# Performance work log

Hardware: AMD Instinct MI355X
Metric: run time of the kernel (lower is better)

Reference implementation:

```python
import jax, jax.numpy as jnp
import numpy as np

COMMITMENT_COST = 0.25
NUM_EMBEDDINGS = 4096
EMBEDDING_DIM = 256


def setup_inputs() -> dict:
    key = jax.random.key(0)
    k1, k2 = jax.random.split(key)
    inputs = jax.random.normal(k1, (32, EMBEDDING_DIM, 2048), dtype=jnp.float32)
    # nn.Embedding weight initialized uniform(-1/K, 1/K)
    codebook = jax.random.uniform(
        k2, (NUM_EMBEDDINGS, EMBEDDING_DIM), dtype=jnp.float32,
        minval=-1.0 / NUM_EMBEDDINGS, maxval=1.0 / NUM_EMBEDDINGS)
    return {"inputs": inputs, "codebook": codebook}


def reference(inputs, codebook):
    B, D, S = inputs.shape
    sg = jax.lax.stop_gradient
    # [B, D, S] -> [B*S, D]
    flat = jnp.transpose(inputs, (0, 2, 1)).reshape(-1, D)
    distances = (jnp.sum(flat ** 2, axis=1, keepdims=True)
                 + jnp.sum(codebook ** 2, axis=1)
                 - 2.0 * flat @ codebook.T)
    encoding_indices = jnp.argmin(distances, axis=1)  # [N]
    # direct gather (same math as one-hot @ codebook)
    quantized = codebook[encoding_indices].reshape(B, S, D)
    quantized = jnp.transpose(quantized, (0, 2, 1))  # [B, D, S]
    e_latent_loss = jnp.mean((sg(quantized) - inputs) ** 2)
    q_latent_loss = jnp.mean((quantized - sg(inputs)) ** 2)
    loss = COMMITMENT_COST * e_latent_loss + q_latent_loss
    # straight-through estimator
    quantized_st = inputs + sg(quantized - inputs)
    return quantized_st, loss
```

## Files before the change

### kernel.cpp

```cpp
#include <hip/hip_runtime.h>

#define K_CODES 4096
#define DIM 256
#define SEQ 2048
#define NTOK 65536

typedef __bf16 bf16x8 __attribute__((ext_vector_type(8)));
typedef float floatx4 __attribute__((ext_vector_type(4)));
typedef unsigned short u16x8 __attribute__((ext_vector_type(8)));

__device__ __forceinline__ unsigned short f2bf(float f) {
    union { float f; unsigned int u; } v; v.f = f;
    unsigned int u = v.u;
    unsigned int r = u + 0x7fffu + ((u >> 16) & 1u);
    return (unsigned short)(r >> 16);
}

__device__ __forceinline__ void async_cp16(const void* g, const void* lds_base) {
    typedef __attribute__((address_space(1))) const unsigned int guint;
    typedef __attribute__((address_space(3))) unsigned int luint;
    __builtin_amdgcn_global_load_lds(
        (guint*)(unsigned long long)g,
        (luint*)(unsigned int)(unsigned long long)lds_base,
        16, 0, 0);
}

__global__ __launch_bounds__(256) void k_prep(const float* __restrict__ cb,
        unsigned short* __restrict__ cb_swz, float* __restrict__ norms,
        float* __restrict__ loss_slot) {
    const int c = blockIdx.x;
    const int t = threadIdx.x;
    const int row_loc = t >> 3;
    const int ks = t & 7;
    const int row = c * 32 + row_loc;
    const float* src = cb + (size_t)row * DIM + ks * 32;
    float vals[32];
    float s = 0.0f;
    #pragma unroll
    for (int i = 0; i < 8; ++i) {
        floatx4 v = *(const floatx4*)(src + i * 4);
        #pragma unroll
        for (int j = 0; j < 4; ++j) { vals[i * 4 + j] = v[j]; s += v[j] * v[j]; }
    }
    const int ns = row_loc >> 4, col = row_loc & 15;
    #pragma unroll
    for (int quad = 0; quad < 4; ++quad) {
        u16x8 p;
        #pragma unroll
        for (int j = 0; j < 8; ++j) p[j] = f2bf(vals[quad * 8 + j]);
        *(u16x8*)(cb_swz + ((size_t)((c * 16 + ns * 8 + ks) * 64 + quad * 16 + col)) * 8) = p;
    }
    s += __shfl_xor(s, 1); s += __shfl_xor(s, 2); s += __shfl_xor(s, 4);
    if (ks == 0) norms[row] = s + 0.25f;
    if (c == 0 && t == 0) *loss_slot = 0.0f;
}

__global__ __launch_bounds__(256, 2) void k_argmin(const float* __restrict__ x,
        const unsigned short* __restrict__ cb_swz, const float* __restrict__ norms,
        unsigned int* __restrict__ halfmin, float* __restrict__ loss_slot) {
    __shared__ __align__(16) unsigned short xs[64 * 264];
    __shared__ __align__(16) unsigned short ring[2][8192];
    __shared__ float wpart[4];
    const int t = threadIdx.x;
    const int lane = t & 63, w = t >> 6;
    const int col = lane & 15, quad = lane >> 4;
    const int bx = blockIdx.x;
    const int h = bx & 1;
    const int tb = (bx >> 1) * 256;
    const int b = tb >> 11, s0 = tb & 2047;
    const float* xin = x + (size_t)b * DIM * SEQ;

    {
        const char* src = (const char*)cb_swz + (size_t)h * 64 * 16384;
        #pragma unroll
        for (int i = 0; i < 4; ++i)
            async_cp16(src + i * 4096 + w * 1024 + lane * 16,
                       (char*)ring[0] + i * 4096 + w * 1024);
    }

    bf16x8 af[4][8];
    float a2 = 0.0f;
    const int dg = t >> 4, sq = (t & 15) * 4;
    for (int ph = 0; ph < 4; ++ph) {
        const int sbase = s0 + ph * 64 + sq;
        for (int i = 0; i < 16; ++i) {
            int d = i * 16 + dg;
            floatx4 v = *(const floatx4*)(xin + (size_t)d * SEQ + sbase);
            a2 += v[0]*v[0] + v[1]*v[1] + v[2]*v[2] + v[3]*v[3];
            #pragma unroll
            for (int j = 0; j < 4; ++j) xs[(sq + j) * 264 + d] = f2bf(-2.0f * v[j]);
        }
        __syncthreads();
        if (w == ph) {
            #pragma unroll
            for (int m = 0; m < 4; ++m)
                #pragma unroll
                for (int ks = 0; ks < 8; ++ks)
                    af[m][ks] = *(const bf16x8*)&xs[(m * 16 + col) * 264
                                                    + quad * 8 + ks * 32];
        }
        __syncthreads();
    }
    #pragma unroll
    for (int off = 1; off < 64; off <<= 1) a2 += __shfl_xor(a2, off);
    if (lane == 0) wpart[w] = a2;
    __syncthreads();
    if (t == 0 && h == 0)
        atomicAdd(loss_slot,
                  (wpart[0] + wpart[1] + wpart[2] + wpart[3]) * (1.25f / 16777216.0f));

    unsigned int minkey[4][4];
    #pragma unroll
    for (int m = 0; m < 4; ++m)
        #pragma unroll
        for (int r = 0; r < 4; ++r) minkey[m][r] = 0xFFFFFFFFu;

    #pragma unroll 1
    for (int c = 0; c < 64; ++c) {
        __syncthreads();
        if (c < 63) {
            const char* src = (const char*)cb_swz + (size_t)(h * 64 + c + 1) * 16384;
            char* dst = (char*)ring[(c + 1) & 1];
            #pragma unroll
            for (int i = 0; i < 4; ++i)
                async_cp16(src + i * 4096 + w * 1024 + lane * 16,
                           dst + i * 4096 + w * 1024);
        }
        const unsigned short* buf = ring[c & 1];
        #pragma unroll
        for (int ns = 0; ns < 2; ++ns) {
            const float nv = norms[(h * 64 + c) * 32 + ns * 16 + col];
            bf16x8 bfrag[8];
            #pragma unroll
            for (int ks = 0; ks < 8; ++ks)
                bfrag[ks] = *(const bf16x8*)&buf[((ns * 8 + ks) * 64 + lane) * 8];
            floatx4 acc[4];
            #pragma unroll
            for (int m = 0; m < 4; ++m) acc[m] = (floatx4){nv, nv, nv, nv};
            #pragma unroll
            for (int ks = 0; ks < 8; ++ks)
                #pragma unroll
                for (int m = 0; m < 4; ++m)
                    acc[m] = __builtin_amdgcn_mfma_f32_16x16x32_bf16(
                                 af[m][ks], bfrag[ks], acc[m], 0, 0, 0);
            const unsigned int code = (unsigned int)((h * 64 + c) * 32 + ns * 16 + col);
            #pragma unroll
            for (int m = 0; m < 4; ++m)
                #pragma unroll
                for (int r = 0; r < 4; ++r) {
                    unsigned int key = (__float_as_uint(acc[m][r]) & 0xFFFFF000u) | code;
                    minkey[m][r] = key < minkey[m][r] ? key : minkey[m][r];
                }
        }
    }

    #pragma unroll
    for (int m = 0; m < 4; ++m)
        #pragma unroll
        for (int r = 0; r < 4; ++r) {
            unsigned int k = minkey[m][r];
            #pragma unroll
            for (int off = 8; off >= 1; off >>= 1) {
                unsigned int o = __shfl_xor(k, off);
                k = o < k ? o : k;
            }
            if (col == 0)
                halfmin[h * NTOK + tb + w * 64 + m * 16 + quad * 4 + r] = k;
        }
}

__global__ __launch_bounds__(256) void k_gather(const float* __restrict__ cb,
        const unsigned int* __restrict__ halfmin, float* __restrict__ out,
        float* __restrict__ loss_slot) {
    __shared__ int sidx[64];
    const int t = threadIdx.x;
    const int tb = blockIdx.x * 64;
    const int b = tb >> 11, s0 = tb & 2047;
    if (t < 64) {
        unsigned int k0 = halfmin[tb + t], k1 = halfmin[NTOK + tb + t];
        unsigned int km = k0 < k1 ? k0 : k1;
        sidx[t] = (int)(km & 0xFFFu);
        float dv = __uint_as_float(km & 0xFFFFF000u) - 0.25f;
        #pragma unroll
        for (int off = 32; off; off >>= 1) dv += __shfl_xor(dv, off);
        if (t == 0) atomicAdd(loss_slot, dv * (1.25f / 16777216.0f));
    }
    __syncthreads();
    const int q = t & 15, dg = t >> 4;
    int rows[4];
    #pragma unroll
    for (int k = 0; k < 4; ++k) rows[k] = sidx[q * 4 + k];
    #pragma unroll
    for (int i = 0; i < 16; ++i) {
        const int d = i * 16 + dg;
        floatx4 v;
        #pragma unroll
        for (int k = 0; k < 4; ++k) v[k] = cb[(size_t)rows[k] * DIM + d];
        *(floatx4*)(out + (size_t)b * DIM * SEQ + (size_t)d * SEQ + s0 + q * 4) = v;
    }
}

extern "C" void kernel_launch(void* const* d_in, const int* in_sizes, int n_in,
                              void* d_out, int out_size, void* d_ws, size_t ws_size,
                              hipStream_t stream) {
    const float* inputs   = (const float*)d_in[0];
    const float* codebook = (const float*)d_in[1];
    float* out = (float*)d_out;
    unsigned short* cb_swz = (unsigned short*)d_ws;
    float* norms = (float*)((char*)d_ws + (size_t)K_CODES * DIM * 2);
    unsigned int* halfmin = (unsigned int*)((char*)d_ws + (size_t)K_CODES * DIM * 2
                                            + K_CODES * 4);
    float* loss_slot = out + (out_size - 1);

    hipLaunchKernelGGL(k_prep,   dim3(K_CODES / 32),     dim3(256), 0, stream,
                       codebook, cb_swz, norms, loss_slot);
    hipLaunchKernelGGL(k_argmin, dim3(NTOK / 256 * 2),   dim3(256), 0, stream,
                       inputs, cb_swz, norms, halfmin, loss_slot);
    hipLaunchKernelGGL(k_gather, dim3(NTOK / 64),        dim3(256), 0, stream,
                       codebook, halfmin, out, loss_slot);
}
```

Measured before the change: 259.8 us.

## Triple-buffer codebook ring with split barriers and staged norms in LDS

Replaces the double-buffered codebook ring in the argmin kernel with a three-stage ring that has two chunks in flight. Explicit vmcnt waits and raw s_barrier calls replace the per-iteration __syncthreads, and s_setprio raises priority around the MFMA blocks. Norms are staged once into shared memory, and the -2x staging tile is halved and XOR-swizzled to cut LDS bank conflicts. The goals are better overlap of global-to-LDS loads with MFMA work and less barrier stall, at the cost of more LDS use and fragile hand-written waitcnt logic.

```diff
diff --git a/kernel.cpp b/kernel.cpp
--- a/kernel.cpp
+++ b/kernel.cpp
@@ -58,8 +58,9 @@
 __global__ __launch_bounds__(256, 2) void k_argmin(const float* __restrict__ x,
         const unsigned short* __restrict__ cb_swz, const float* __restrict__ norms,
         unsigned int* __restrict__ halfmin, float* __restrict__ loss_slot) {
-    __shared__ __align__(16) unsigned short xs[64 * 264];
-    __shared__ __align__(16) unsigned short ring[2][8192];
+    __shared__ __align__(16) unsigned short xs[32 * 264];
+    __shared__ __align__(16) unsigned short ring3[3][8192];
+    __shared__ __align__(16) float norms_s[2048];
     __shared__ float wpart[4];
     const int t = threadIdx.x;
     const int lane = t & 63, w = t >> 6;
@@ -73,31 +74,45 @@
     {
         const char* src = (const char*)cb_swz + (size_t)h * 64 * 16384;
         #pragma unroll
-        for (int i = 0; i < 4; ++i)
-            async_cp16(src + i * 4096 + w * 1024 + lane * 16,
-                       (char*)ring[0] + i * 4096 + w * 1024);
+        for (int cc = 0; cc < 2; ++cc)
+            #pragma unroll
+            for (int i = 0; i < 4; ++i)
+                async_cp16(src + cc * 16384 + i * 4096 + w * 1024 + lane * 16,
+                           (char*)ring3[cc] + i * 4096 + w * 1024);
+    }
+    {
+        const float* ng = norms + h * 2048;
+        *(floatx4*)&norms_s[t * 8]     = *(const floatx4*)(ng + t * 8);
+        *(floatx4*)&norms_s[t * 8 + 4] = *(const floatx4*)(ng + t * 8 + 4);
     }
 
     bf16x8 af[4][8];
     float a2 = 0.0f;
-    const int dg = t >> 4, sq = (t & 15) * 4;
-    for (int ph = 0; ph < 4; ++ph) {
-        const int sbase = s0 + ph * 64 + sq;
-        for (int i = 0; i < 16; ++i) {
-            int d = i * 16 + dg;
+    const int q = t & 7, dgp = t >> 3, sq = q * 4;
+    for (int p = 0; p < 8; ++p) {
+        const int sbase = s0 + p * 32 + sq;
+        #pragma unroll
+        for (int i = 0; i < 8; ++i) {
+            const int d = i * 32 + dgp;
             floatx4 v = *(const floatx4*)(xin + (size_t)d * SEQ + sbase);
             a2 += v[0]*v[0] + v[1]*v[1] + v[2]*v[2] + v[3]*v[3];
-            #pragma unroll
-            for (int j = 0; j < 4; ++j) xs[(sq + j) * 264 + d] = f2bf(-2.0f * v[j]);
+            const int chs = (d >> 3) ^ q;
+            #pragma unroll
+            for (int j = 0; j < 4; ++j)
+                xs[(sq + j) * 264 + chs * 8 + (d & 7)] = f2bf(-2.0f * v[j]);
         }
         __syncthreads();
-        if (w == ph) {
-            #pragma unroll
-            for (int m = 0; m < 4; ++m)
+        if ((p >> 1) == w) {
+            const int mm = (p & 1) * 2;
+            #pragma unroll
+            for (int m2 = 0; m2 < 2; ++m2) {
+                const int row = m2 * 16 + col;
+                const int swz = (row >> 2) & 7;
                 #pragma unroll
                 for (int ks = 0; ks < 8; ++ks)
-                    af[m][ks] = *(const bf16x8*)&xs[(m * 16 + col) * 264
-                                                    + quad * 8 + ks * 32];
+                    af[mm + m2][ks] = *(const bf16x8*)
+                        &xs[row * 264 + ((quad + ks * 4) ^ swz) * 8];
+            }
         }
         __syncthreads();
     }
@@ -115,43 +130,77 @@
         #pragma unroll
         for (int r = 0; r < 4; ++r) minkey[m][r] = 0xFFFFFFFFu;
 
+    const unsigned short* rcur = ring3[0];
+    const unsigned short* rnxt = ring3[1];
+    const unsigned short* rstg = ring3[2];
+    const char* srcp = (const char*)cb_swz + ((size_t)h * 64 + 2) * 16384;
+    const float* np = norms_s + col;
+    unsigned int codev = (unsigned int)(h * 64 * 32 + col);
+
     #pragma unroll 1
     for (int c = 0; c < 64; ++c) {
-        __syncthreads();
-        if (c < 63) {
-            const char* src = (const char*)cb_swz + (size_t)(h * 64 + c + 1) * 16384;
-            char* dst = (char*)ring[(c + 1) & 1];
+        float nv0 = np[0];
+        bf16x8 bf0[8];
+        #pragma unroll
+        for (int ks = 0; ks < 8; ++ks)
+            bf0[ks] = *(const bf16x8*)&rcur[(ks * 64 + lane) * 8];
+        if (c < 62) {
             #pragma unroll
             for (int i = 0; i < 4; ++i)
-                async_cp16(src + i * 4096 + w * 1024 + lane * 16,
-                           dst + i * 4096 + w * 1024);
-        }
-        const unsigned short* buf = ring[c & 1];
-        #pragma unroll
-        for (int ns = 0; ns < 2; ++ns) {
-            const float nv = norms[(h * 64 + c) * 32 + ns * 16 + col];
-            bf16x8 bfrag[8];
-            #pragma unroll
-            for (int ks = 0; ks < 8; ++ks)
-                bfrag[ks] = *(const bf16x8*)&buf[((ns * 8 + ks) * 64 + lane) * 8];
-            floatx4 acc[4];
-            #pragma unroll
-            for (int m = 0; m < 4; ++m) acc[m] = (floatx4){nv, nv, nv, nv};
-            #pragma unroll
-            for (int ks = 0; ks < 8; ++ks)
-                #pragma unroll
-                for (int m = 0; m < 4; ++m)
-                    acc[m] = __builtin_amdgcn_mfma_f32_16x16x32_bf16(
-                                 af[m][ks], bfrag[ks], acc[m], 0, 0, 0);
-            const unsigned int code = (unsigned int)((h * 64 + c) * 32 + ns * 16 + col);
+                async_cp16(srcp + i * 4096 + w * 1024 + lane * 16,
+                           (const char*)rstg + i * 4096 + w * 1024);
+        }
+        __builtin_amdgcn_s_barrier();
+        asm volatile("s_waitcnt lgkmcnt(0)" ::: "memory");
+        __builtin_amdgcn_s_setprio(1);
+        floatx4 acc0[4];
+        #pragma unroll
+        for (int m = 0; m < 4; ++m) acc0[m] = (floatx4){nv0, nv0, nv0, nv0};
+        #pragma unroll
+        for (int ks = 0; ks < 8; ++ks)
             #pragma unroll
             for (int m = 0; m < 4; ++m)
-                #pragma unroll
-                for (int r = 0; r < 4; ++r) {
-                    unsigned int key = (__float_as_uint(acc[m][r]) & 0xFFFFF000u) | code;
-                    minkey[m][r] = key < minkey[m][r] ? key : minkey[m][r];
-                }
-        }
+                acc0[m] = __builtin_amdgcn_mfma_f32_16x16x32_bf16(
+                              af[m][ks], bf0[ks], acc0[m], 0, 0, 0);
+        __builtin_amdgcn_s_setprio(0);
+        float nv1 = np[16];
+        bf16x8 bf1[8];
+        #pragma unroll
+        for (int ks = 0; ks < 8; ++ks)
+            bf1[ks] = *(const bf16x8*)&rcur[((8 + ks) * 64 + lane) * 8];
+        #pragma unroll
+        for (int m = 0; m < 4; ++m)
+            #pragma unroll
+            for (int r = 0; r < 4; ++r) {
+                unsigned int key = (__float_as_uint(acc0[m][r]) & 0xFFFFF000u) | codev;
+                minkey[m][r] = key < minkey[m][r] ? key : minkey[m][r];
+            }
+        __builtin_amdgcn_s_barrier();
+        asm volatile("s_waitcnt lgkmcnt(0)" ::: "memory");
+        __builtin_amdgcn_s_setprio(1);
+        floatx4 acc1[4];
+        #pragma unroll
+        for (int m = 0; m < 4; ++m) acc1[m] = (floatx4){nv1, nv1, nv1, nv1};
+        #pragma unroll
+        for (int ks = 0; ks < 8; ++ks)
+            #pragma unroll
+            for (int m = 0; m < 4; ++m)
+                acc1[m] = __builtin_amdgcn_mfma_f32_16x16x32_bf16(
+                              af[m][ks], bf1[ks], acc1[m], 0, 0, 0);
+        __builtin_amdgcn_s_setprio(0);
+        #pragma unroll
+        for (int m = 0; m < 4; ++m)
+            #pragma unroll
+            for (int r = 0; r < 4; ++r) {
+                unsigned int key = (__float_as_uint(acc1[m][r]) & 0xFFFFF000u)
+                                   | (codev + 16);
+                minkey[m][r] = key < minkey[m][r] ? key : minkey[m][r];
+            }
+        if (c < 62) asm volatile("s_waitcnt vmcnt(4)" ::: "memory");
+        else        asm volatile("s_waitcnt vmcnt(0)" ::: "memory");
+        __builtin_amdgcn_s_barrier();
+        const unsigned short* tmp = rcur; rcur = rnxt; rnxt = rstg; rstg = tmp;
+        srcp += 16384; np += 32; codev += 32;
     }
 
     #pragma unroll
```

Result: slower. 282.3 us (+8.6%).

## Switch argmin to 32x32x16 MFMA with swizzled LDS, norms in LDS, staged gather

Applied to the files above, without the earlier changes.

The distance kernel moves from 16x16x32 to 32x32x16 bf16 MFMA tiles. The codebook swizzle and the per-wave A fragments (two 32-token tiles) are rebuilt to match, and the x staging buffer in LDS gets XOR swizzling to avoid bank conflicts. Codebook norms are preloaded into LDS, the block index is remapped so the two codebook halves are scheduled apart, and MFMA sections are raised with s_setprio. The gather kernel now stages whole codebook rows in LDS for coalesced reads before the transposed write. The larger tiles cut LDS B-fragment traffic per FLOP, at the cost of more registers per wave and more complex index mapping.

```diff
diff --git a/kernel.cpp b/kernel.cpp
--- a/kernel.cpp
+++ b/kernel.cpp
@@ -7,6 +7,8 @@
 
 typedef __bf16 bf16x8 __attribute__((ext_vector_type(8)));
 typedef float floatx4 __attribute__((ext_vector_type(4)));
+typedef float floatx2 __attribute__((ext_vector_type(2)));
+typedef float floatx16 __attribute__((ext_vector_type(16)));
 typedef unsigned short u16x8 __attribute__((ext_vector_type(8)));
 
 __device__ __forceinline__ unsigned short f2bf(float f) {
@@ -28,12 +30,12 @@
 __global__ __launch_bounds__(256) void k_prep(const float* __restrict__ cb,
         unsigned short* __restrict__ cb_swz, float* __restrict__ norms,
         float* __restrict__ loss_slot) {
-    const int c = blockIdx.x;
+    const int gc = blockIdx.x;
     const int t = threadIdx.x;
-    const int row_loc = t >> 3;
-    const int ks = t & 7;
-    const int row = c * 32 + row_loc;
-    const float* src = cb + (size_t)row * DIM + ks * 32;
+    const int colc = t >> 3;
+    const int o = t & 7;
+    const int row = gc * 32 + colc;
+    const float* src = cb + (size_t)row * DIM + o * 32;
     float vals[32];
     float s = 0.0f;
     #pragma unroll
@@ -42,31 +44,34 @@
         #pragma unroll
         for (int j = 0; j < 4; ++j) { vals[i * 4 + j] = v[j]; s += v[j] * v[j]; }
     }
-    const int ns = row_loc >> 4, col = row_loc & 15;
-    #pragma unroll
-    for (int quad = 0; quad < 4; ++quad) {
+    #pragma unroll
+    for (int q4 = 0; q4 < 4; ++q4) {
+        const int g8 = o * 4 + q4;
+        const int ks = g8 >> 1, kh = g8 & 1;
         u16x8 p;
         #pragma unroll
-        for (int j = 0; j < 8; ++j) p[j] = f2bf(vals[quad * 8 + j]);
-        *(u16x8*)(cb_swz + ((size_t)((c * 16 + ns * 8 + ks) * 64 + quad * 16 + col)) * 8) = p;
+        for (int j = 0; j < 8; ++j) p[j] = f2bf(vals[q4 * 8 + j]);
+        *(u16x8*)(cb_swz + ((size_t)(gc * 16 + ks) * 64 + kh * 32 + colc) * 8) = p;
     }
     s += __shfl_xor(s, 1); s += __shfl_xor(s, 2); s += __shfl_xor(s, 4);
-    if (ks == 0) norms[row] = s + 0.25f;
-    if (c == 0 && t == 0) *loss_slot = 0.0f;
+    if (o == 0) norms[row] = s + 0.25f;
+    if (gc == 0 && t == 0) *loss_slot = 0.0f;
 }
 
 __global__ __launch_bounds__(256, 2) void k_argmin(const float* __restrict__ x,
         const unsigned short* __restrict__ cb_swz, const float* __restrict__ norms,
         unsigned int* __restrict__ halfmin, float* __restrict__ loss_slot) {
-    __shared__ __align__(16) unsigned short xs[64 * 264];
+    __shared__ __align__(16) unsigned short xs[32 * 264];
     __shared__ __align__(16) unsigned short ring[2][8192];
+    __shared__ __align__(16) float norms_s[2048];
     __shared__ float wpart[4];
     const int t = threadIdx.x;
     const int lane = t & 63, w = t >> 6;
-    const int col = lane & 15, quad = lane >> 4;
-    const int bx = blockIdx.x;
-    const int h = bx & 1;
-    const int tb = (bx >> 1) * 256;
+    const int col32 = lane & 31, kh = lane >> 5;
+    const int bid = blockIdx.x;
+    const int tbid = (bid & 7) * 32 + (bid >> 4);
+    const int h = (bid >> 3) & 1;
+    const int tb = tbid * 256;
     const int b = tb >> 11, s0 = tb & 2047;
     const float* xin = x + (size_t)b * DIM * SEQ;
 
@@ -77,27 +82,43 @@
             async_cp16(src + i * 4096 + w * 1024 + lane * 16,
                        (char*)ring[0] + i * 4096 + w * 1024);
     }
-
-    bf16x8 af[4][8];
+    {
+        const float* ng = norms + h * 2048;
+        *(floatx4*)&norms_s[t * 8]     = *(const floatx4*)(ng + t * 8);
+        *(floatx4*)&norms_s[t * 8 + 4] = *(const floatx4*)(ng + t * 8 + 4);
+    }
+
+    bf16x8 af0[16], af1[16];
     float a2 = 0.0f;
-    const int dg = t >> 4, sq = (t & 15) * 4;
-    for (int ph = 0; ph < 4; ++ph) {
-        const int sbase = s0 + ph * 64 + sq;
-        for (int i = 0; i < 16; ++i) {
-            int d = i * 16 + dg;
+    const int q = t & 7, dgp = t >> 3, sq = q * 4;
+    #pragma unroll
+    for (int p = 0; p < 8; ++p) {
+        const int sbase = s0 + p * 32 + sq;
+        #pragma unroll
+        for (int i = 0; i < 8; ++i) {
+            const int d = i * 32 + dgp;
             floatx4 v = *(const floatx4*)(xin + (size_t)d * SEQ + sbase);
             a2 += v[0]*v[0] + v[1]*v[1] + v[2]*v[2] + v[3]*v[3];
-            #pragma unroll
-            for (int j = 0; j < 4; ++j) xs[(sq + j) * 264 + d] = f2bf(-2.0f * v[j]);
-        }
-        __syncthreads();
-        if (w == ph) {
-            #pragma unroll
-            for (int m = 0; m < 4; ++m)
+            const int chs = (d >> 3) ^ q;
+            #pragma unroll
+            for (int j = 0; j < 4; ++j)
+                xs[(sq + j) * 264 + chs * 8 + (d & 7)] = f2bf(-2.0f * v[j]);
+        }
+        __syncthreads();
+        if ((p >> 1) == w) {
+            const int tok = col32;
+            const int swz = tok >> 2;
+            if ((p & 1) == 0) {
                 #pragma unroll
-                for (int ks = 0; ks < 8; ++ks)
-                    af[m][ks] = *(const bf16x8*)&xs[(m * 16 + col) * 264
-                                                    + quad * 8 + ks * 32];
+                for (int ks = 0; ks < 16; ++ks)
+                    af0[ks] = *(const bf16x8*)
+                        &xs[tok * 264 + ((ks * 2 + kh) ^ swz) * 8];
+            } else {
+                #pragma unroll
+                for (int ks = 0; ks < 16; ++ks)
+                    af1[ks] = *(const bf16x8*)
+                        &xs[tok * 264 + ((ks * 2 + kh) ^ swz) * 8];
+            }
         }
         __syncthreads();
     }
@@ -109,69 +130,77 @@
         atomicAdd(loss_slot,
                   (wpart[0] + wpart[1] + wpart[2] + wpart[3]) * (1.25f / 16777216.0f));
 
-    unsigned int minkey[4][4];
-    #pragma unroll
-    for (int m = 0; m < 4; ++m)
-        #pragma unroll
-        for (int r = 0; r < 4; ++r) minkey[m][r] = 0xFFFFFFFFu;
+    unsigned int minkey0[16], minkey1[16];
+    #pragma unroll
+    for (int r = 0; r < 16; ++r) { minkey0[r] = 0xFFFFFFFFu; minkey1[r] = 0xFFFFFFFFu; }
 
     #pragma unroll 1
     for (int c = 0; c < 64; ++c) {
         __syncthreads();
         if (c < 63) {
-            const char* src = (const char*)cb_swz + (size_t)(h * 64 + c + 1) * 16384;
+            const char* srcp = (const char*)cb_swz + ((size_t)(h * 64) + c + 1) * 16384;
             char* dst = (char*)ring[(c + 1) & 1];
             #pragma unroll
             for (int i = 0; i < 4; ++i)
-                async_cp16(src + i * 4096 + w * 1024 + lane * 16,
+                async_cp16(srcp + i * 4096 + w * 1024 + lane * 16,
                            dst + i * 4096 + w * 1024);
         }
         const unsigned short* buf = ring[c & 1];
-        #pragma unroll
-        for (int ns = 0; ns < 2; ++ns) {
-            const float nv = norms[(h * 64 + c) * 32 + ns * 16 + col];
-            bf16x8 bfrag[8];
-            #pragma unroll
-            for (int ks = 0; ks < 8; ++ks)
-                bfrag[ks] = *(const bf16x8*)&buf[((ns * 8 + ks) * 64 + lane) * 8];
-            floatx4 acc[4];
-            #pragma unroll
-            for (int m = 0; m < 4; ++m) acc[m] = (floatx4){nv, nv, nv, nv};
-            #pragma unroll
-            for (int ks = 0; ks < 8; ++ks)
-                #pragma unroll
-                for (int m = 0; m < 4; ++m)
-                    acc[m] = __builtin_amdgcn_mfma_f32_16x16x32_bf16(
-                                 af[m][ks], bfrag[ks], acc[m], 0, 0, 0);
-            const unsigned int code = (unsigned int)((h * 64 + c) * 32 + ns * 16 + col);
-            #pragma unroll
-            for (int m = 0; m < 4; ++m)
-                #pragma unroll
-                for (int r = 0; r < 4; ++r) {
-                    unsigned int key = (__float_as_uint(acc[m][r]) & 0xFFFFF000u) | code;
-                    minkey[m][r] = key < minkey[m][r] ? key : minkey[m][r];
-                }
-        }
-    }
-
-    #pragma unroll
-    for (int m = 0; m < 4; ++m)
-        #pragma unroll
-        for (int r = 0; r < 4; ++r) {
-            unsigned int k = minkey[m][r];
-            #pragma unroll
-            for (int off = 8; off >= 1; off >>= 1) {
-                unsigned int o = __shfl_xor(k, off);
-                k = o < k ? o : k;
+        const float nv = norms_s[c * 32 + col32];
+        floatx16 acc0, acc1;
+        #pragma unroll
+        for (int r = 0; r < 16; ++r) { acc0[r] = nv; acc1[r] = nv; }
+        #pragma unroll
+        for (int hf = 0; hf < 2; ++hf) {
+            bf16x8 bfr[8];
+            #pragma unroll
+            for (int kk = 0; kk < 8; ++kk)
+                bfr[kk] = *(const bf16x8*)&buf[((hf * 8 + kk) * 64 + lane) * 8];
+            __builtin_amdgcn_s_setprio(1);
+            #pragma unroll
+            for (int kk = 0; kk < 8; ++kk) {
+                acc0 = __builtin_amdgcn_mfma_f32_32x32x16_bf16(
+                           af0[hf * 8 + kk], bfr[kk], acc0, 0, 0, 0);
+                acc1 = __builtin_amdgcn_mfma_f32_32x32x16_bf16(
+                           af1[hf * 8 + kk], bfr[kk], acc1, 0, 0, 0);
             }
-            if (col == 0)
-                halfmin[h * NTOK + tb + w * 64 + m * 16 + quad * 4 + r] = k;
-        }
+            __builtin_amdgcn_s_setprio(0);
+        }
+        const unsigned int code = (unsigned int)((h * 64 + c) * 32) | (unsigned int)col32;
+        #pragma unroll
+        for (int r = 0; r < 16; ++r) {
+            unsigned int k0 = (__float_as_uint(acc0[r]) & 0xFFFFF000u) | code;
+            minkey0[r] = k0 < minkey0[r] ? k0 : minkey0[r];
+            unsigned int k1 = (__float_as_uint(acc1[r]) & 0xFFFFF000u) | code;
+            minkey1[r] = k1 < minkey1[r] ? k1 : minkey1[r];
+        }
+    }
+
+    #pragma unroll
+    for (int r = 0; r < 16; ++r) {
+        unsigned int k = minkey0[r];
+        #pragma unroll
+        for (int off = 16; off >= 1; off >>= 1) {
+            unsigned int o = __shfl_xor(k, off);
+            k = o < k ? o : k;
+        }
+        if (col32 == 0)
+            halfmin[h * NTOK + tb + w * 64 + (r & 3) + 8 * (r >> 2) + 4 * kh] = k;
+        unsigned int k2 = minkey1[r];
+        #pragma unroll
+        for (int off = 16; off >= 1; off >>= 1) {
+            unsigned int o = __shfl_xor(k2, off);
+            k2 = o < k2 ? o : k2;
+        }
+        if (col32 == 0)
+            halfmin[h * NTOK + tb + w * 64 + 32 + (r & 3) + 8 * (r >> 2) + 4 * kh] = k2;
+    }
 }
 
 __global__ __launch_bounds__(256) void k_gather(const float* __restrict__ cb,
         const unsigned int* __restrict__ halfmin, float* __restrict__ out,
         float* __restrict__ loss_slot) {
+    __shared__ float rows_s[32 * 258];
     __shared__ int sidx[64];
     const int t = threadIdx.x;
     const int tb = blockIdx.x * 64;
@@ -186,17 +215,26 @@
         if (t == 0) atomicAdd(loss_slot, dv * (1.25f / 16777216.0f));
     }
     __syncthreads();
-    const int q = t & 15, dg = t >> 4;
-    int rows[4];
-    #pragma unroll
-    for (int k = 0; k < 4; ++k) rows[k] = sidx[q * 4 + k];
-    #pragma unroll
-    for (int i = 0; i < 16; ++i) {
-        const int d = i * 16 + dg;
-        floatx4 v;
-        #pragma unroll
-        for (int k = 0; k < 4; ++k) v[k] = cb[(size_t)rows[k] * DIM + d];
-        *(floatx4*)(out + (size_t)b * DIM * SEQ + (size_t)d * SEQ + s0 + q * 4) = v;
+    const int r = t >> 3, cs = (t & 7) * 32;
+    const int qg = t & 7, dgb = t >> 3;
+    #pragma unroll 1
+    for (int p = 0; p < 2; ++p) {
+        if (p) __syncthreads();
+        const float* srcr = cb + (size_t)sidx[p * 32 + r] * DIM + cs;
+        float* dstr = &rows_s[r * 258 + cs];
+        #pragma unroll
+        for (int i2 = 0; i2 < 16; ++i2)
+            *(floatx2*)(dstr + i2 * 2) = *(const floatx2*)(srcr + i2 * 2);
+        __syncthreads();
+        #pragma unroll
+        for (int i = 0; i < 8; ++i) {
+            const int d = i * 32 + dgb;
+            floatx4 v;
+            #pragma unroll
+            for (int k = 0; k < 4; ++k) v[k] = rows_s[(qg * 4 + k) * 258 + d];
+            *(floatx4*)(out + (size_t)b * DIM * SEQ + (size_t)d * SEQ
+                        + s0 + p * 32 + qg * 4) = v;
+        }
     }
 }
 
```

Measured after the change: 329.3 us. 26.7% more time.

## Fuse gather into argmin kernel via atomic-min merge and last-block epilogue

Applied to the files above, without the earlier changes.

Removes the separate gather kernel. Each half-codebook block now atomicMin's its per-token keys into a shared merged array, and the second block to finish, detected with a counter, performs the loss accumulation and the transposed codebook gather through LDS. It also stages norms in LDS, XOR-swizzles the xs tile to reduce bank conflicts, and remaps block ids so the two halves of a token tile are scheduled apart. In exchange it adds atomics, threadfence and counter overhead, plus a more serialized tail in the finishing blocks.

```diff
diff --git a/kernel.cpp b/kernel.cpp
--- a/kernel.cpp
+++ b/kernel.cpp
@@ -27,6 +27,7 @@
 
 __global__ __launch_bounds__(256) void k_prep(const float* __restrict__ cb,
         unsigned short* __restrict__ cb_swz, float* __restrict__ norms,
+        unsigned int* __restrict__ merged, unsigned int* __restrict__ counters,
         float* __restrict__ loss_slot) {
     const int c = blockIdx.x;
     const int t = threadIdx.x;
@@ -52,21 +53,34 @@
     }
     s += __shfl_xor(s, 1); s += __shfl_xor(s, 2); s += __shfl_xor(s, 4);
     if (ks == 0) norms[row] = s + 0.25f;
-    if (c == 0 && t == 0) *loss_slot = 0.0f;
+    const int g = c * 256 + t;
+    *(unsigned long long*)(merged + 2 * g) = 0xFFFFFFFFFFFFFFFFull;
+    if (g < 256) counters[g] = 0u;
+    if (g == 0) *loss_slot = 0.0f;
 }
 
 __global__ __launch_bounds__(256, 2) void k_argmin(const float* __restrict__ x,
-        const unsigned short* __restrict__ cb_swz, const float* __restrict__ norms,
-        unsigned int* __restrict__ halfmin, float* __restrict__ loss_slot) {
-    __shared__ __align__(16) unsigned short xs[64 * 264];
-    __shared__ __align__(16) unsigned short ring[2][8192];
-    __shared__ float wpart[4];
+        const unsigned short* __restrict__ cb_swz, const float* __restrict__ cb,
+        const float* __restrict__ norms, unsigned int* __restrict__ merged,
+        unsigned int* __restrict__ counters, float* __restrict__ out,
+        float* __restrict__ loss_slot) {
+    __shared__ __align__(16) char smem[57880];
+    unsigned short* xs = (unsigned short*)smem;
+    unsigned short* ring0 = (unsigned short*)(smem + 16896);
+    unsigned short* ring1 = (unsigned short*)(smem + 33280);
+    float* norms_s = (float*)(smem + 49664);
+    float* wpart = (float*)(smem + 57856);
+    int* flag_s = (int*)(smem + 57872);
+    float* rows_s = (float*)smem;
+    int* sidx_s = (int*)(smem + 33024);
+
     const int t = threadIdx.x;
     const int lane = t & 63, w = t >> 6;
     const int col = lane & 15, quad = lane >> 4;
-    const int bx = blockIdx.x;
-    const int h = bx & 1;
-    const int tb = (bx >> 1) * 256;
+    const int bid = blockIdx.x;
+    const int tbid = (bid & 7) * 32 + (bid >> 4);
+    const int h = (bid >> 3) & 1;
+    const int tb = tbid * 256;
     const int b = tb >> 11, s0 = tb & 2047;
     const float* xin = x + (size_t)b * DIM * SEQ;
 
@@ -75,29 +89,41 @@
         #pragma unroll
         for (int i = 0; i < 4; ++i)
             async_cp16(src + i * 4096 + w * 1024 + lane * 16,
-                       (char*)ring[0] + i * 4096 + w * 1024);
+                       (char*)ring0 + i * 4096 + w * 1024);
+    }
+    {
+        const float* ng = norms + h * 2048;
+        *(floatx4*)&norms_s[t * 8]     = *(const floatx4*)(ng + t * 8);
+        *(floatx4*)&norms_s[t * 8 + 4] = *(const floatx4*)(ng + t * 8 + 4);
     }
 
     bf16x8 af[4][8];
     float a2 = 0.0f;
-    const int dg = t >> 4, sq = (t & 15) * 4;
-    for (int ph = 0; ph < 4; ++ph) {
-        const int sbase = s0 + ph * 64 + sq;
-        for (int i = 0; i < 16; ++i) {
-            int d = i * 16 + dg;
+    const int q = t & 7, dgp = t >> 3, sq = q * 4;
+    for (int p = 0; p < 8; ++p) {
+        const int sbase = s0 + p * 32 + sq;
+        #pragma unroll
+        for (int i = 0; i < 8; ++i) {
+            const int d = i * 32 + dgp;
             floatx4 v = *(const floatx4*)(xin + (size_t)d * SEQ + sbase);
             a2 += v[0]*v[0] + v[1]*v[1] + v[2]*v[2] + v[3]*v[3];
-            #pragma unroll
-            for (int j = 0; j < 4; ++j) xs[(sq + j) * 264 + d] = f2bf(-2.0f * v[j]);
-        }
-        __syncthreads();
-        if (w == ph) {
-            #pragma unroll
-            for (int m = 0; m < 4; ++m)
+            const int chs = (d >> 3) ^ q;
+            #pragma unroll
+            for (int j = 0; j < 4; ++j)
+                xs[(sq + j) * 264 + chs * 8 + (d & 7)] = f2bf(-2.0f * v[j]);
+        }
+        __syncthreads();
+        if ((p >> 1) == w) {
+            const int mm = (p & 1) * 2;
+            #pragma unroll
+            for (int m2 = 0; m2 < 2; ++m2) {
+                const int row = m2 * 16 + col;
+                const int swz = (row >> 2) & 7;
                 #pragma unroll
                 for (int ks = 0; ks < 8; ++ks)
-                    af[m][ks] = *(const bf16x8*)&xs[(m * 16 + col) * 264
-                                                    + quad * 8 + ks * 32];
+                    af[mm + m2][ks] = *(const bf16x8*)
+                        &xs[row * 264 + ((quad + ks * 4) ^ swz) * 8];
+            }
         }
         __syncthreads();
     }
@@ -119,17 +145,17 @@
     for (int c = 0; c < 64; ++c) {
         __syncthreads();
         if (c < 63) {
-            const char* src = (const char*)cb_swz + (size_t)(h * 64 + c + 1) * 16384;
-            char* dst = (char*)ring[(c + 1) & 1];
+            const char* srcp = (const char*)cb_swz + ((size_t)(h * 64) + c + 1) * 16384;
+            char* dst = (char*)(((c + 1) & 1) ? ring1 : ring0);
             #pragma unroll
             for (int i = 0; i < 4; ++i)
-                async_cp16(src + i * 4096 + w * 1024 + lane * 16,
+                async_cp16(srcp + i * 4096 + w * 1024 + lane * 16,
                            dst + i * 4096 + w * 1024);
         }
-        const unsigned short* buf = ring[c & 1];
+        const unsigned short* buf = (c & 1) ? ring1 : ring0;
         #pragma unroll
         for (int ns = 0; ns < 2; ++ns) {
-            const float nv = norms[(h * 64 + c) * 32 + ns * 16 + col];
+            const float nv = norms_s[c * 32 + ns * 16 + col];
             bf16x8 bfrag[8];
             #pragma unroll
             for (int ks = 0; ks < 8; ++ks)
@@ -165,38 +191,46 @@
                 k = o < k ? o : k;
             }
             if (col == 0)
-                halfmin[h * NTOK + tb + w * 64 + m * 16 + quad * 4 + r] = k;
-        }
-}
-
-__global__ __launch_bounds__(256) void k_gather(const float* __restrict__ cb,
-        const unsigned int* __restrict__ halfmin, float* __restrict__ out,
-        float* __restrict__ loss_slot) {
-    __shared__ int sidx[64];
-    const int t = threadIdx.x;
-    const int tb = blockIdx.x * 64;
-    const int b = tb >> 11, s0 = tb & 2047;
-    if (t < 64) {
-        unsigned int k0 = halfmin[tb + t], k1 = halfmin[NTOK + tb + t];
-        unsigned int km = k0 < k1 ? k0 : k1;
-        sidx[t] = (int)(km & 0xFFFu);
-        float dv = __uint_as_float(km & 0xFFFFF000u) - 0.25f;
-        #pragma unroll
-        for (int off = 32; off; off >>= 1) dv += __shfl_xor(dv, off);
-        if (t == 0) atomicAdd(loss_slot, dv * (1.25f / 16777216.0f));
-    }
-    __syncthreads();
-    const int q = t & 15, dg = t >> 4;
-    int rows[4];
-    #pragma unroll
-    for (int k = 0; k < 4; ++k) rows[k] = sidx[q * 4 + k];
-    #pragma unroll
-    for (int i = 0; i < 16; ++i) {
-        const int d = i * 16 + dg;
-        floatx4 v;
-        #pragma unroll
-        for (int k = 0; k < 4; ++k) v[k] = cb[(size_t)rows[k] * DIM + d];
-        *(floatx4*)(out + (size_t)b * DIM * SEQ + (size_t)d * SEQ + s0 + q * 4) = v;
+                atomicMin(&merged[tb + w * 64 + m * 16 + quad * 4 + r], k);
+        }
+
+    __threadfence();
+    if (t == 0) flag_s[0] = (atomicAdd(&counters[tbid], 1u) == 1u) ? 1 : 0;
+    __syncthreads();
+    if (!flag_s[0]) return;
+
+    unsigned int kk = atomicMin(&merged[tb + t], 0xFFFFFFFFu);
+    float dv = __uint_as_float(kk & 0xFFFFF000u) - 0.25f;
+    #pragma unroll
+    for (int off = 1; off < 64; off <<= 1) dv += __shfl_xor(dv, off);
+    __syncthreads();
+    sidx_s[t] = (int)(kk & 0xFFFu);
+    if (lane == 0) wpart[w] = dv;
+    __syncthreads();
+    if (t == 0)
+        atomicAdd(loss_slot,
+                  (wpart[0] + wpart[1] + wpart[2] + wpart[3]) * (1.25f / 16777216.0f));
+
+    const int rr = t >> 3, cs8 = (t & 7) * 32;
+    const int qg = t & 7, dgb = t >> 3;
+    #pragma unroll 1
+    for (int p = 0; p < 8; ++p) {
+        if (p) __syncthreads();
+        const float* srcr = cb + (size_t)sidx_s[p * 32 + rr] * DIM + cs8;
+        float* dstr = rows_s + rr * 258 + cs8;
+        #pragma unroll
+        for (int i4 = 0; i4 < 8; ++i4)
+            *(floatx4*)(dstr + i4 * 4) = *(const floatx4*)(srcr + i4 * 4);
+        __syncthreads();
+        #pragma unroll
+        for (int i = 0; i < 8; ++i) {
+            const int d = i * 32 + dgb;
+            floatx4 v;
+            #pragma unroll
+            for (int k2 = 0; k2 < 4; ++k2) v[k2] = rows_s[(qg * 4 + k2) * 258 + d];
+            *(floatx4*)(out + (size_t)b * DIM * SEQ + (size_t)d * SEQ
+                        + s0 + p * 32 + qg * 4) = v;
+        }
     }
 }
 
@@ -208,14 +242,13 @@
     float* out = (float*)d_out;
     unsigned short* cb_swz = (unsigned short*)d_ws;
     float* norms = (float*)((char*)d_ws + (size_t)K_CODES * DIM * 2);
-    unsigned int* halfmin = (unsigned int*)((char*)d_ws + (size_t)K_CODES * DIM * 2
-                                            + K_CODES * 4);
+    unsigned int* merged = (unsigned int*)((char*)d_ws + (size_t)K_CODES * DIM * 2
+                                           + K_CODES * 4);
+    unsigned int* counters = merged + NTOK;
     float* loss_slot = out + (out_size - 1);
 
-    hipLaunchKernelGGL(k_prep,   dim3(K_CODES / 32),     dim3(256), 0, stream,
-                       codebook, cb_swz, norms, loss_slot);
-    hipLaunchKernelGGL(k_argmin, dim3(NTOK / 256 * 2),   dim3(256), 0, stream,
-                       inputs, cb_swz, norms, halfmin, loss_slot);
-    hipLaunchKernelGGL(k_gather, dim3(NTOK / 64),        dim3(256), 0, stream,
-                       codebook, halfmin, out, loss_slot);
-}
+    hipLaunchKernelGGL(k_prep,   dim3(K_CODES / 32),   dim3(256), 0, stream,
+                       codebook, cb_swz, norms, merged, counters, loss_slot);
+    hipLaunchKernelGGL(k_argmin, dim3(NTOK / 256 * 2), dim3(256), 0, stream,
+                       inputs, cb_swz, codebook, norms, merged, counters, out, loss_slot);
+}
```

Measured after the change: 776.6 us. 199% more time.
